# Kernel optimization log

Hardware: AMD Instinct MI355X
Metric: run time of the kernel (lower is better)

Reference implementation:

```python
import jax, jax.numpy as jnp
import numpy as np
from jax import lax

# 5x5 Gaussian kernel, sigma=1.0 (matches cv2.getGaussianKernel(5, 1.0))
_xs = np.arange(5) - 2
_k1 = np.exp(-(_xs ** 2) / 2.0)
_k1 = (_k1 / _k1.sum()).astype(np.float32)
_K2 = jnp.asarray(np.outer(_k1, _k1))  # [5,5]


def _blur(x):
    """Gaussian blur on [B,H,W] with BORDER_REFLECT_101 (cv2 default)."""
    xp = jnp.pad(x, ((0, 0), (2, 2), (2, 2)), mode='reflect')
    y = lax.conv_general_dilated(xp[:, None], _K2[None, None], (1, 1), 'VALID')
    return y[:, 0]


def _hist_entropy(noise):
    """Per-image 50-bin histogram entropy over range (-0.5, 0.5). noise: [B,H,W]."""
    def one(v):
        h, _ = jnp.histogram(v, bins=50, range=(-0.5, 0.5))
        h = h.astype(jnp.float32)
        p = h / (h.sum() + 1e-10)
        return -jnp.sum(p * jnp.log2(p + 1e-10))
    return jax.vmap(one)(noise.reshape(noise.shape[0], -1))


def _noise_features(x):
    # x: [B,3,H,W] float in [0,1]
    # gray path: quantize to uint8 (truncation), cv2 RGB2GRAY weights w/ rounding
    xq = jnp.floor(jnp.clip(x * 255.0, 0.0, 255.0))  # uint8 truncation
    gray = jnp.round(0.299 * xq[:, 0] + 0.587 * xq[:, 1] + 0.114 * xq[:, 2]) / 255.0
    noise = gray - _blur(gray)  # [B,H,W]
    local_var = jnp.var(noise, axis=(1, 2))
    noise_std = jnp.std(noise, axis=(1, 2))
    entropy = _hist_entropy(noise)
    # per-channel noise std on the float image (no quantization in original)
    B, C, H, W = x.shape
    ch = x.reshape(B * C, H, W)
    ch_noise = ch - _blur(ch)
    ch_std = jnp.std(ch_noise, axis=(1, 2)).reshape(B, C)
    return jnp.stack([local_var, noise_std, entropy], axis=1).astype(jnp.float32)\
        , ch_std


def setup_inputs() -> dict:
    key = jax.random.key(0)
    ks = jax.random.split(key, 5)
    B, H, W = 64, 512, 512
    x = jax.random.uniform(ks[0], (B, 3, H, W), dtype=jnp.float32)
    # torch Linear weights: [out, in], kaiming-uniform-ish init
    W1 = jax.random.uniform(ks[1], (32, 6), minval=-1, maxval=1) / np.sqrt(6)
    b1 = jax.random.uniform(ks[2], (32,), minval=-1, maxval=1) / np.sqrt(6)
    W2 = jax.random.uniform(ks[3], (64, 32), minval=-1, maxval=1) / np.sqrt(32)
    b2 = jax.random.uniform(ks[4], (64,), minval=-1, maxval=1) / np.sqrt(32)
    return {"x": x, "W1": W1, "b1": b1, "W2": W2, "b2": b2}


def reference(x, W1, b1, W2, b2):
    stats, ch_std = _noise_features(x)
    feats = jnp.concatenate([stats, ch_std], axis=1)  # [B,6]
    h = jax.nn.relu(feats @ W1.T + b1)  # dropout in eval mode = identity
    return jax.nn.relu(h @ W2.T + b2)
```

## Files before the change

kernel.cpp:

```cpp
#include <hip/hip_runtime.h>
#include <math.h>

#define HH 512
#define WW 512
#define NB 64
#define CH_STRIDE (HH*WW)
#define IMG_STRIDE (3*CH_STRIDE)

#define GK0 0.0544886846f
#define GK1 0.2442013419f
#define GK2 0.4026199468f

__device__ __forceinline__ float quant255(float v) {
    return floorf(fminf(fmaxf(__fmul_rn(v, 255.0f), 0.0f), 255.0f));
}
__device__ __forceinline__ float gray255(float qa, float qb, float qc) {
    return rintf(__fadd_rn(__fadd_rn(__fmul_rn(0.299f, qa), __fmul_rn(0.587f, qb)),
                           __fmul_rn(0.114f, qc)));
}

__global__ __launch_bounds__(256, 2)
void noise_main(const float* __restrict__ x, float* __restrict__ gsums,
                unsigned int* __restrict__ ghist)
{
    __shared__ unsigned int lhist[4][2][50];
    const int tid  = threadIdx.x;
    const int lane = tid & 63;
    const int wid  = tid >> 6;
    for (int i = tid; i < 400; i += 256) ((unsigned int*)lhist)[i] = 0u;
    __syncthreads();

    const int rawblk = blockIdx.x;
    const int blk = (rawblk & 7) * 64 + (rawblk >> 3);

    const int b     = blk >> 3;
    const int strip = (blk >> 2) & 1;
    const int cg    = blk & 3;
    const int chunk = cg * 4 + wid;
    const int R0    = chunk * 32;
    const int X0    = strip * 256;
    const int gcol  = X0 + lane * 4;

    const int cLo = (gcol == 0)   ? 0   : gcol - 4;
    const int cHi = (gcol == 508) ? 504 : gcol + 4;

    const float* pa = x + (size_t)b * IMG_STRIDE;
    const float* pb = pa + CH_STRIDE;
    const float* pc = pb + CH_STRIDE;

    float hrA[5][4], hrB[5][4], hrC[5][4], hrG[5][4];
    float d1A[4]={0,0,0,0}, d1B[4]={0,0,0,0}, d1C[4]={0,0,0,0}, d1G[4]={0,0,0,0};
    float d2A[4]={0,0,0,0}, d2B[4]={0,0,0,0}, d2C[4]={0,0,0,0}, d2G[4]={0,0,0,0};
    float sA=0.f,qA=0.f,sB=0.f,qB=0.f,sC=0.f,qC=0.f,sG=0.f,qG=0.f;

    float4 va, vb, vc, vLa, vLb, vLc, vRa, vRb, vRc;
    float4 nva, nvb, nvc, nvLa, nvLb, nvLc, nvRa, nvRb, nvRc;

#define LOADROW(T, VA_,VB_,VC_, LA_,LB_,LC_, RA_,RB_,RC_) do {                  \
        int r_ = R0 - 2 + (T);                                                  \
        r_ = (r_ < 0) ? -r_ : ((r_ >= HH) ? (2*(HH-1) - r_) : r_);              \
        const int ro_ = r_ * WW;                                                \
        VA_ = *(const float4*)(pa + ro_ + gcol);                                \
        VB_ = *(const float4*)(pb + ro_ + gcol);                                \
        VC_ = *(const float4*)(pc + ro_ + gcol);                                \
        LA_ = *(const float4*)(pa + ro_ + cLo);                                 \
        LB_ = *(const float4*)(pb + ro_ + cLo);                                 \
        LC_ = *(const float4*)(pc + ro_ + cLo);                                 \
        RA_ = *(const float4*)(pa + ro_ + cHi);                                 \
        RB_ = *(const float4*)(pb + ro_ + cHi);                                 \
        RC_ = *(const float4*)(pc + ro_ + cHi);                                 \
    } while (0)

    LOADROW(0, va,vb,vc, vLa,vLb,vLc, vRa,vRb,vRc);

    #pragma unroll 1
    for (int tb = 0; tb < 8; ++tb) {
        #pragma unroll
        for (int u = 0; u < 5; ++u) {
            const int t = tb * 5 + u;
            if (t < 36) {
                if (t + 1 < 36)
                    LOADROW(t + 1, nva,nvb,nvc, nvLa,nvLb,nvLc, nvRa,nvRb,nvRc);

                float g0 = gray255(quant255(va.x), quant255(vb.x), quant255(vc.x));
                float g1 = gray255(quant255(va.y), quant255(vb.y), quant255(vc.y));
                float g2 = gray255(quant255(va.z), quant255(vb.z), quant255(vc.z));
                float g3 = gray255(quant255(va.w), quant255(vb.w), quant255(vc.w));

                float l2a = vLa.z, l1a = vLa.w, r0a = vRa.x, r1a = vRa.y;
                float l2b = vLb.z, l1b = vLb.w, r0b = vRb.x, r1b = vRb.y;
                float l2c = vLc.z, l1c = vLc.w, r0c = vRc.x, r1c = vRc.y;
                float gl2 = __shfl_up(g2, 1),   gl1 = __shfl_up(g3, 1);
                float gr0 = __shfl_down(g0, 1), gr1 = __shfl_down(g1, 1);

                if (lane == 0) {
                    if (X0 == 0) {
                        l2a = va.z; l1a = va.y; l2b = vb.z; l1b = vb.y; l2c = vc.z; l1c = vc.y;
                        gl2 = g2;   gl1 = g1;
                    } else {
                        gl2 = gray255(quant255(vLa.z), quant255(vLb.z), quant255(vLc.z));
                        gl1 = gray255(quant255(vLa.w), quant255(vLb.w), quant255(vLc.w));
                    }
                }
                if (lane == 63) {
                    if (X0 == 0) {
                        gr0 = gray255(quant255(vRa.x), quant255(vRb.x), quant255(vRc.x));
                        gr1 = gray255(quant255(vRa.y), quant255(vRb.y), quant255(vRc.y));
                    } else {
                        r0a = va.z; r1a = va.y; r0b = vb.z; r1b = vb.y; r0c = vc.z; r1c = vc.y;
                        gr0 = g2;   gr1 = g1;
                    }
                }

                hrA[u][0] = GK0*(l2a+va.z) + GK1*(l1a+va.y) + GK2*va.x;
                hrA[u][1] = GK0*(l1a+va.w) + GK1*(va.x+va.z) + GK2*va.y;
                hrA[u][2] = GK0*(va.x+r0a) + GK1*(va.y+va.w) + GK2*va.z;
                hrA[u][3] = GK0*(va.y+r1a) + GK1*(va.z+r0a) + GK2*va.w;
                hrB[u][0] = GK0*(l2b+vb.z) + GK1*(l1b+vb.y) + GK2*vb.x;
                hrB[u][1] = GK0*(l1b+vb.w) + GK1*(vb.x+vb.z) + GK2*vb.y;
                hrB[u][2] = GK0*(vb.x+r0b) + GK1*(vb.y+vb.w) + GK2*vb.z;
                hrB[u][3] = GK0*(vb.y+r1b) + GK1*(vb.z+r0b) + GK2*vb.w;
                hrC[u][0] = GK0*(l2c+vc.z) + GK1*(l1c+vc.y) + GK2*vc.x;
                hrC[u][1] = GK0*(l1c+vc.w) + GK1*(vc.x+vc.z) + GK2*vc.y;
                hrC[u][2] = GK0*(vc.x+r0c) + GK1*(vc.y+vc.w) + GK2*vc.z;
                hrC[u][3] = GK0*(vc.y+r1c) + GK1*(vc.z+r0c) + GK2*vc.w;
                hrG[u][0] = GK0*(gl2+g2) + GK1*(gl1+g1) + GK2*g0;
                hrG[u][1] = GK0*(gl1+g3) + GK1*(g0+g2)  + GK2*g1;
                hrG[u][2] = GK0*(g0+gr0) + GK1*(g1+g3)  + GK2*g2;
                hrG[u][3] = GK0*(g1+gr1) + GK1*(g2+gr0) + GK2*g3;

                if (t >= 4) {
                    const int s0=(u+1)%5, s1=(u+2)%5, s2=(u+3)%5, s3=(u+4)%5, s4=u;
                    #pragma unroll
                    for (int j = 0; j < 4; ++j) {
                        float bl, v;
                        bl = GK0*(hrA[s0][j]+hrA[s4][j]) + GK1*(hrA[s1][j]+hrA[s3][j]) + GK2*hrA[s2][j];
                        v  = d2A[j] - bl;  sA += v;  qA = fmaf(v, v, qA);
                        bl = GK0*(hrB[s0][j]+hrB[s4][j]) + GK1*(hrB[s1][j]+hrB[s3][j]) + GK2*hrB[s2][j];
                        v  = d2B[j] - bl;  sB += v;  qB = fmaf(v, v, qB);
                        bl = GK0*(hrC[s0][j]+hrC[s4][j]) + GK1*(hrC[s1][j]+hrC[s3][j]) + GK2*hrC[s2][j];
                        v  = d2C[j] - bl;  sC += v;  qC = fmaf(v, v, qC);
                        bl = GK0*(hrG[s0][j]+hrG[s4][j]) + GK1*(hrG[s1][j]+hrG[s3][j]) + GK2*hrG[s2][j];
                        v  = d2G[j] - bl;  sG += v;  qG = fmaf(v, v, qG);
                        if (v >= -127.5f && v <= 127.5f) {
                            int idx = (int)((v + 127.5f) * 0.19607843137254902f);
                            idx = idx > 49 ? 49 : idx;
                            atomicAdd(&lhist[wid][lane & 1][idx], 1u);
                        }
                    }
                }

                #pragma unroll
                for (int j = 0; j < 4; ++j) { d2A[j]=d1A[j]; d2B[j]=d1B[j]; d2C[j]=d1C[j]; d2G[j]=d1G[j]; }
                d1A[0]=va.x; d1A[1]=va.y; d1A[2]=va.z; d1A[3]=va.w;
                d1B[0]=vb.x; d1B[1]=vb.y; d1B[2]=vb.z; d1B[3]=vb.w;
                d1C[0]=vc.x; d1C[1]=vc.y; d1C[2]=vc.z; d1C[3]=vc.w;
                d1G[0]=g0;   d1G[1]=g1;   d1G[2]=g2;   d1G[3]=g3;

                va  = nva;  vb  = nvb;  vc  = nvc;
                vLa = nvLa; vLb = nvLb; vLc = nvLc;
                vRa = nvRa; vRb = nvRb; vRc = nvRc;
            }
        }
    }
#undef LOADROW

    float acc[8] = {sA, qA, sB, qB, sC, qC, sG, qG};
    #pragma unroll
    for (int f = 0; f < 8; ++f) {
        float v = acc[f];
        #pragma unroll
        for (int o = 32; o > 0; o >>= 1) v += __shfl_down(v, o);
        if (lane == 0) atomicAdd(&gsums[b*8 + f], v);
    }
    __syncthreads();
    if (tid < 50) {
        unsigned int h = lhist[0][0][tid] + lhist[0][1][tid]
                       + lhist[1][0][tid] + lhist[1][1][tid]
                       + lhist[2][0][tid] + lhist[2][1][tid]
                       + lhist[3][0][tid] + lhist[3][1][tid];
        atomicAdd(&ghist[b*50 + tid], h);
    }
}

__global__ __launch_bounds__(64)
void noise_final(const float* __restrict__ gsums, const unsigned int* __restrict__ ghist,
                 const float* __restrict__ W1, const float* __restrict__ b1,
                 const float* __restrict__ W2, const float* __restrict__ b2,
                 float* __restrict__ out)
{
    const int b = threadIdx.x;
    if (b >= NB) return;
    const float invN = 1.0f / (float)(HH*WW);
    float feats[6];
    {
        float s = gsums[b*8 + 6], q = gsums[b*8 + 7];
        float m = s * invN;
        float var255 = q * invN - m*m;
        var255 = var255 < 0.f ? 0.f : var255;
        float var = var255 * (1.0f/65025.0f);
        feats[0] = var; feats[1] = sqrtf(var);
    }
    {
        float tot = 0.f;
        for (int i = 0; i < 50; ++i) tot += (float)ghist[b*50 + i];
        float inv = 1.0f / (tot + 1e-10f);
        float e = 0.f;
        for (int i = 0; i < 50; ++i) {
            float p = (float)ghist[b*50 + i] * inv;
            e -= p * log2f(p + 1e-10f);
        }
        feats[2] = e;
    }
    for (int c = 0; c < 3; ++c) {
        float s = gsums[b*8 + 2*c], q = gsums[b*8 + 2*c + 1];
        float m = s * invN;
        float v = q * invN - m*m;
        feats[3+c] = sqrtf(v < 0.f ? 0.f : v);
    }
    float h[32];
    #pragma unroll
    for (int i = 0; i < 32; ++i) {
        float a = b1[i];
        #pragma unroll
        for (int j = 0; j < 6; ++j) a = fmaf(feats[j], W1[i*6 + j], a);
        h[i] = a > 0.f ? a : 0.f;
    }
    for (int k = 0; k < 64; ++k) {
        float a = b2[k];
        #pragma unroll
        for (int j = 0; j < 32; ++j) a = fmaf(h[j], W2[k*32 + j], a);
        out[b*64 + k] = a > 0.f ? a : 0.f;
    }
}

extern "C" void kernel_launch(void* const* d_in, const int* in_sizes, int n_in,
                              void* d_out, int out_size, void* d_ws, size_t ws_size,
                              hipStream_t stream) {
    (void)in_sizes; (void)n_in; (void)out_size; (void)ws_size;
    const float* x  = (const float*)d_in[0];
    const float* W1 = (const float*)d_in[1];
    const float* b1 = (const float*)d_in[2];
    const float* W2 = (const float*)d_in[3];
    const float* b2 = (const float*)d_in[4];
    float* out = (float*)d_out;

    float* gsums = (float*)d_ws;
    unsigned int* ghist = (unsigned int*)((char*)d_ws + NB*8*4);
    hipMemsetAsync(d_ws, 0, NB*8*4 + NB*50*4, stream);

    hipLaunchKernelGGL(noise_main, dim3(512), dim3(256), 0, stream, x, gsums, ghist);
    hipLaunchKernelGGL(noise_final, dim3(1), dim3(64), 0, stream,
                       gsums, ghist, W1, b1, W2, b2, out);
}
```

Baseline: 324.4 us.

## Prefetch two rows ahead, shrink halo loads to float2, widen histogram privatization

The row loop now prefetches two rows ahead instead of one, which gives more memory-level parallelism to hide global load latency. The left and right halo loads are narrowed from float4 to float2, since only two neighbour elements per side are used, which cuts redundant load traffic. The shared histogram is split four ways by lane instead of two to reduce LDS atomic contention. In exchange, register pressure rises from the extra prefetch buffers, which could hurt occupancy under launch_bounds(256,2).

```diff
diff --git a/kernel.cpp b/kernel.cpp
--- a/kernel.cpp
+++ b/kernel.cpp
@@ -23,11 +23,11 @@
 void noise_main(const float* __restrict__ x, float* __restrict__ gsums,
                 unsigned int* __restrict__ ghist)
 {
-    __shared__ unsigned int lhist[4][2][50];
+    __shared__ unsigned int lhist[4][4][50];
     const int tid  = threadIdx.x;
     const int lane = tid & 63;
     const int wid  = tid >> 6;
-    for (int i = tid; i < 400; i += 256) ((unsigned int*)lhist)[i] = 0u;
+    for (int i = tid; i < 800; i += 256) ((unsigned int*)lhist)[i] = 0u;
     __syncthreads();
 
     const int rawblk = blockIdx.x;
@@ -41,7 +41,7 @@
     const int X0    = strip * 256;
     const int gcol  = X0 + lane * 4;
 
-    const int cLo = (gcol == 0)   ? 0   : gcol - 4;
+    const int cLo = (gcol == 0)   ? 0   : gcol - 2;
     const int cHi = (gcol == 508) ? 504 : gcol + 4;
 
     const float* pa = x + (size_t)b * IMG_STRIDE;
@@ -53,8 +53,9 @@
     float d2A[4]={0,0,0,0}, d2B[4]={0,0,0,0}, d2C[4]={0,0,0,0}, d2G[4]={0,0,0,0};
     float sA=0.f,qA=0.f,sB=0.f,qB=0.f,sC=0.f,qC=0.f,sG=0.f,qG=0.f;
 
-    float4 va, vb, vc, vLa, vLb, vLc, vRa, vRb, vRc;
-    float4 nva, nvb, nvc, nvLa, nvLb, nvLc, nvRa, nvRb, nvRc;
+    float4 va, vb, vc;       float2 La, Lb, Lc, Ra, Rb, Rc;
+    float4 nva, nvb, nvc;    float2 nLa, nLb, nLc, nRa, nRb, nRc;
+    float4 mva, mvb, mvc;    float2 mLa, mLb, mLc, mRa, mRb, mRc;
 
 #define LOADROW(T, VA_,VB_,VC_, LA_,LB_,LC_, RA_,RB_,RC_) do {                  \
         int r_ = R0 - 2 + (T);                                                  \
@@ -63,15 +64,16 @@
         VA_ = *(const float4*)(pa + ro_ + gcol);                                \
         VB_ = *(const float4*)(pb + ro_ + gcol);                                \
         VC_ = *(const float4*)(pc + ro_ + gcol);                                \
-        LA_ = *(const float4*)(pa + ro_ + cLo);                                 \
-        LB_ = *(const float4*)(pb + ro_ + cLo);                                 \
-        LC_ = *(const float4*)(pc + ro_ + cLo);                                 \
-        RA_ = *(const float4*)(pa + ro_ + cHi);                                 \
-        RB_ = *(const float4*)(pb + ro_ + cHi);                                 \
-        RC_ = *(const float4*)(pc + ro_ + cHi);                                 \
+        LA_ = *(const float2*)(pa + ro_ + cLo);                                 \
+        LB_ = *(const float2*)(pb + ro_ + cLo);                                 \
+        LC_ = *(const float2*)(pc + ro_ + cLo);                                 \
+        RA_ = *(const float2*)(pa + ro_ + cHi);                                 \
+        RB_ = *(const float2*)(pb + ro_ + cHi);                                 \
+        RC_ = *(const float2*)(pc + ro_ + cHi);                                 \
     } while (0)
 
-    LOADROW(0, va,vb,vc, vLa,vLb,vLc, vRa,vRb,vRc);
+    LOADROW(0, va,vb,vc,    La,Lb,Lc,    Ra,Rb,Rc);
+    LOADROW(1, nva,nvb,nvc, nLa,nLb,nLc, nRa,nRb,nRc);
 
     #pragma unroll 1
     for (int tb = 0; tb < 8; ++tb) {
@@ -79,17 +81,17 @@
         for (int u = 0; u < 5; ++u) {
             const int t = tb * 5 + u;
             if (t < 36) {
-                if (t + 1 < 36)
-                    LOADROW(t + 1, nva,nvb,nvc, nvLa,nvLb,nvLc, nvRa,nvRb,nvRc);
+                if (t + 2 < 36)
+                    LOADROW(t + 2, mva,mvb,mvc, mLa,mLb,mLc, mRa,mRb,mRc);
 
                 float g0 = gray255(quant255(va.x), quant255(vb.x), quant255(vc.x));
                 float g1 = gray255(quant255(va.y), quant255(vb.y), quant255(vc.y));
                 float g2 = gray255(quant255(va.z), quant255(vb.z), quant255(vc.z));
                 float g3 = gray255(quant255(va.w), quant255(vb.w), quant255(vc.w));
 
-                float l2a = vLa.z, l1a = vLa.w, r0a = vRa.x, r1a = vRa.y;
-                float l2b = vLb.z, l1b = vLb.w, r0b = vRb.x, r1b = vRb.y;
-                float l2c = vLc.z, l1c = vLc.w, r0c = vRc.x, r1c = vRc.y;
+                float l2a = La.x, l1a = La.y, r0a = Ra.x, r1a = Ra.y;
+                float l2b = Lb.x, l1b = Lb.y, r0b = Rb.x, r1b = Rb.y;
+                float l2c = Lc.x, l1c = Lc.y, r0c = Rc.x, r1c = Rc.y;
                 float gl2 = __shfl_up(g2, 1),   gl1 = __shfl_up(g3, 1);
                 float gr0 = __shfl_down(g0, 1), gr1 = __shfl_down(g1, 1);
 
@@ -98,14 +100,14 @@
                         l2a = va.z; l1a = va.y; l2b = vb.z; l1b = vb.y; l2c = vc.z; l1c = vc.y;
                         gl2 = g2;   gl1 = g1;
                     } else {
-                        gl2 = gray255(quant255(vLa.z), quant255(vLb.z), quant255(vLc.z));
-                        gl1 = gray255(quant255(vLa.w), quant255(vLb.w), quant255(vLc.w));
+                        gl2 = gray255(quant255(La.x), quant255(Lb.x), quant255(Lc.x));
+                        gl1 = gray255(quant255(La.y), quant255(Lb.y), quant255(Lc.y));
                     }
                 }
                 if (lane == 63) {
                     if (X0 == 0) {
-                        gr0 = gray255(quant255(vRa.x), quant255(vRb.x), quant255(vRc.x));
-                        gr1 = gray255(quant255(vRa.y), quant255(vRb.y), quant255(vRc.y));
+                        gr0 = gray255(quant255(Ra.x), quant255(Rb.x), quant255(Rc.x));
+                        gr1 = gray255(quant255(Ra.y), quant255(Rb.y), quant255(Rc.y));
                     } else {
                         r0a = va.z; r1a = va.y; r0b = vb.z; r1b = vb.y; r0c = vc.z; r1c = vc.y;
                         gr0 = g2;   gr1 = g1;
@@ -145,7 +147,7 @@
                         if (v >= -127.5f && v <= 127.5f) {
                             int idx = (int)((v + 127.5f) * 0.19607843137254902f);
                             idx = idx > 49 ? 49 : idx;
-                            atomicAdd(&lhist[wid][lane & 1][idx], 1u);
+                            atomicAdd(&lhist[wid][lane & 3][idx], 1u);
                         }
                     }
                 }
@@ -157,9 +159,10 @@
                 d1C[0]=vc.x; d1C[1]=vc.y; d1C[2]=vc.z; d1C[3]=vc.w;
                 d1G[0]=g0;   d1G[1]=g1;   d1G[2]=g2;   d1G[3]=g3;
 
-                va  = nva;  vb  = nvb;  vc  = nvc;
-                vLa = nvLa; vLb = nvLb; vLc = nvLc;
-                vRa = nvRa; vRb = nvRb; vRc = nvRc;
+                va = nva;  vb = nvb;  vc = nvc;
+                La = nLa;  Lb = nLb;  Lc = nLc;  Ra = nRa;  Rb = nRb;  Rc = nRc;
+                nva = mva; nvb = mvb; nvc = mvc;
+                nLa = mLa; nLb = mLb; nLc = mLc; nRa = mRa; nRb = mRb; nRc = mRc;
             }
         }
     }
@@ -175,10 +178,11 @@
     }
     __syncthreads();
     if (tid < 50) {
-        unsigned int h = lhist[0][0][tid] + lhist[0][1][tid]
-                       + lhist[1][0][tid] + lhist[1][1][tid]
-                       + lhist[2][0][tid] + lhist[2][1][tid]
-                       + lhist[3][0][tid] + lhist[3][1][tid];
+        unsigned int h = 0;
+        #pragma unroll
+        for (int w = 0; w < 4; ++w)
+            #pragma unroll
+            for (int p = 0; p < 4; ++p) h += lhist[w][p][tid];
         atomicAdd(&ghist[b*50 + tid], h);
     }
 }
```

Result: no change. 328.5 us (+1.2%).
